# Performance work log

Measured on AMD Instinct MI355X. Metric: run time of the kernel, lower is better.

## Reference

```python
import jax, jax.numpy as jnp
import numpy as np

B, S, H, D, R = 16, 2048, 1024, 64, 2048  # batch, seq_len, hidden, inner_dim, num_relations


def setup_inputs() -> dict:
    key = jax.random.key(0)
    k1, k2, k3, k4 = jax.random.split(key, 4)
    last_hidden_state = jax.random.normal(k1, (B, S, H), dtype=jnp.float32)
    W = jax.random.normal(k2, (H, 2 * D), dtype=jnp.float32) * (H ** -0.5)
    b = jnp.zeros((2 * D,), dtype=jnp.float32)
    position_ids = jnp.tile(jnp.arange(S, dtype=jnp.int32), (B, 1))
    relations_idx = jax.random.randint(k3, (B, R, 4), 0, S, dtype=jnp.int32)
    labels_mask = (jax.random.uniform(k4, (B, R)) > 0.1).astype(jnp.float32)
    return {
        'last_hidden_state': last_hidden_state,
        'W': W,
        'b': b,
        'position_ids': position_ids,
        'relations_idx': relations_idx,
        'labels_mask': labels_mask,
    }


def reference(last_hidden_state, W, b, position_ids, relations_idx, labels_mask):
    # linear projection -> split into q/k halves
    outputs = last_hidden_state @ W + b            # [B,S,2D]
    qw, kw = outputs[..., :D], outputs[..., D:]    # each [B,S,D]

    # RoPE (interleaved sin/cos layout matching torch stack+reshape)
    inv_freq = jnp.power(10000.0, -2.0 * jnp.arange(D // 2, dtype=jnp.float32) / D)
    ang = position_ids[..., None].astype(jnp.float32) * inv_freq  # [B,S,D/2]
    sin_pos = jnp.repeat(jnp.sin(ang), 2, axis=-1)  # [B,S,D]
    cos_pos = jnp.repeat(jnp.cos(ang), 2, axis=-1)  # [B,S,D]

    def rotate(x):
        x2 = jnp.stack([-x[..., 1::2], x[..., ::2]], axis=-1).reshape(x.shape)
        return x * cos_pos + x2 * sin_pos

    qw = rotate(qw)
    kw = rotate(kw)

    # gather span endpoints: relations_idx[...,k] -> [B,R], take along seq axis
    def gather(x, idx):
        return jnp.take_along_axis(x, idx[..., None], axis=1)  # [B,R,D]

    sub_qw = jnp.concatenate([gather(qw, relations_idx[:, :, 0]),
                              gather(qw, relations_idx[:, :, 1])], axis=-1)  # [B,R,2D]
    obj_kw = jnp.concatenate([gather(kw, relations_idx[:, :, 2]),
                              gather(kw, relations_idx[:, :, 3])], axis=-1)  # [B,R,2D]

    logits = jnp.sum(sub_qw * obj_kw, axis=-1)     # [B,R]
    logits = logits + (1.0 - labels_mask) * -1e12
    return logits / jnp.sqrt(jnp.float32(D))
```

## Files before the change

### kernel.cpp

```cpp
#include <hip/hip_runtime.h>
#include <hip/hip_bf16.h>
#include <cstdint>

#define B_ 16
#define S_ 2048
#define H_ 1024
#define D_ 64
#define R_ 2048
#define M_ (B_*S_)
#define N_ 128
#define NC_ 16

typedef short short8 __attribute__((ext_vector_type(8)));
typedef float f32x4  __attribute__((ext_vector_type(4)));

__device__ __forceinline__ unsigned short f2bf(float f) {
    unsigned u = __builtin_bit_cast(unsigned, f);
    u += 0x7FFFu + ((u >> 16) & 1u);
    return (unsigned short)(u >> 16);
}
__device__ __forceinline__ unsigned pk2(float a, float b) {
    return (unsigned)f2bf(a) | ((unsigned)f2bf(b) << 16);
}
__device__ __forceinline__ float bflo(unsigned u) {
    return __builtin_bit_cast(float, u << 16);
}
__device__ __forceinline__ float bfhi(unsigned u) {
    return __builtin_bit_cast(float, u & 0xFFFF0000u);
}

typedef const __attribute__((address_space(1))) void gvoid_t;
typedef __attribute__((address_space(3))) void lvoid_t;
__device__ __forceinline__ void gload16(const void* g, void* l) {
    __builtin_amdgcn_global_load_lds((gvoid_t*)g, (lvoid_t*)l, 16, 0, 0);
}

__global__ void build_wt(const float* __restrict__ W, unsigned short* __restrict__ Wt) {
    __shared__ float tile[16][128];
    const int tid = threadIdx.x;
    const int k0  = blockIdx.x * 16;
    #pragma unroll
    for (int i = 0; i < 8; i++) {
        const int k = i * 2 + (tid >> 7);
        tile[k][tid & 127] = W[(size_t)(k0 + k) * N_ + (tid & 127)];
    }
    __syncthreads();
    const int n  = tid >> 1;
    const int kh = (tid & 1) * 8;
    short8 v;
    #pragma unroll
    for (int e = 0; e < 8; e++) v[e] = (short)f2bf(tile[kh + e][n]);
    *(short8*)(Wt + (size_t)n * 1024 + k0 + kh) = v;
}

__launch_bounds__(256, 2)
__global__ void gemm_rope(const float* __restrict__ A,
                          const unsigned short* __restrict__ Wt,
                          const float* __restrict__ bias,
                          const int* __restrict__ pos_ids,
                          unsigned* __restrict__ qk)
{
    __shared__ __align__(16) float          abuf[2][64 * 64];
    __shared__ __align__(16) unsigned short wbuf[2][N_ * 64];

    const int tid  = threadIdx.x;
    const int wave = tid >> 6, lane = tid & 63;
    const int ln15 = lane & 15, quad = lane >> 4, key = ln15 & 7;
    const int m0   = blockIdx.x * 64;

    const float* a_g[4];
    const unsigned short* w_g[4];
    int a_lo[4], w_lo[4];
    #pragma unroll
    for (int t = 0; t < 4; t++) {
        const int rl = wave * 16 + t * 4 + (lane >> 4);
        a_g[t]  = A + (size_t)(m0 + rl) * H_ + (((lane & 15) ^ (rl & 7)) << 2);
        a_lo[t] = (wave * 16 + t * 4) * 64;
        const int n = (wave * 4 + t) * 8 + (lane >> 3);
        w_g[t]  = Wt + (size_t)n * 1024 + (((lane & 7) ^ (n & 7)) << 3);
        w_lo[t] = (wave * 4 + t) * 8 * 64;
    }

    f32x4 acc[8];
    #pragma unroll
    for (int j = 0; j < 8; j++) acc[j] = (f32x4)0.f;

    #pragma unroll
    for (int t = 0; t < 4; t++) {
        gload16(a_g[t], &abuf[0][a_lo[t]]);
        gload16(w_g[t], &wbuf[0][w_lo[t]]);
    }

    const float* ab_lane_base;
    for (int kc = 0; kc < NC_; kc++) {
        __syncthreads();
        if (kc + 1 < NC_) {
            const int nb = (kc + 1) & 1;
            #pragma unroll
            for (int t = 0; t < 4; t++) {
                gload16(a_g[t] + (kc + 1) * 64, &abuf[nb][a_lo[t]]);
                gload16(w_g[t] + (kc + 1) * 64, &wbuf[nb][w_lo[t]]);
            }
        }
        const int cb = kc & 1;
        ab_lane_base = &abuf[cb][(wave * 16 + ln15) * 64];
        #pragma unroll
        for (int ks = 0; ks < 2; ks++) {
            const int g0 = ks * 8 + quad * 2;
            f32x4 r0 = *(const f32x4*)(ab_lane_base + ((g0 ^ key) << 2));
            f32x4 r1 = *(const f32x4*)(ab_lane_base + (((g0 + 1) ^ key) << 2));
            int4 ai;
            ai.x = (int)pk2(r0[0], r0[1]);
            ai.y = (int)pk2(r0[2], r0[3]);
            ai.z = (int)pk2(r1[0], r1[1]);
            ai.w = (int)pk2(r1[2], r1[3]);
            const short8 af = __builtin_bit_cast(short8, ai);
            const int p = ((ks * 4 + quad) ^ key) << 3;
            #pragma unroll
            for (int j = 0; j < 8; j++) {
                const short8 bf = *(const short8*)(&wbuf[cb][(j * 16 + ln15) * 64 + p]);
                acc[j] = __builtin_amdgcn_mfma_f32_16x16x32_bf16(af, bf, acc[j], 0, 0, 0);
            }
        }
    }

    const int rbase = m0 + wave * 16 + quad * 4;
    float bv[8], invr[4];
    #pragma unroll
    for (int j = 0; j < 8; j++) bv[j] = bias[j * 16 + ln15];
    #pragma unroll
    for (int jj = 0; jj < 4; jj++) {
        const float fi = (float)((jj * 16 + ln15) >> 1);
        invr[jj] = exp2f(fi * -0.41524101186092029f) * 0.15915494309189535f;
    }
    const bool odd = (ln15 & 1);
    #pragma unroll
    for (int reg = 0; reg < 4; reg++) {
        const int r = rbase + reg;
        const float pos = (float)pos_ids[r];
        float s_[4], c_[4];
        #pragma unroll
        for (int jj = 0; jj < 4; jj++) {
            const float fr = __builtin_amdgcn_fractf(pos * invr[jj]);
            s_[jj] = __builtin_amdgcn_sinf(fr);
            c_[jj] = __builtin_amdgcn_cosf(fr);
        }
        #pragma unroll
        for (int j = 0; j < 8; j++) {
            const int c = j * 16 + ln15;
            float v = acc[j][reg] + bv[j];
            float p = __shfl_xor(v, 1, 64);
            float outv = odd ? fmaf(v, c_[j & 3], p * s_[j & 3])
                             : fmaf(v, c_[j & 3], -p * s_[j & 3]);
            float po = __shfl_xor(outv, 1, 64);
            if (!odd)
                qk[(size_t)r * 64 + (c >> 1)] = pk2(outv, po);
        }
    }
}

__global__ void gather_dot(const unsigned* __restrict__ qk, const int* __restrict__ rel,
                           const float* __restrict__ mask, float* __restrict__ out)
{
    const int t    = blockIdx.x * 256 + threadIdx.x;
    const int w    = t >> 4;
    const int sub  = threadIdx.x & 15;
    const int b    = w >> 11;
    const int4 id4 = ((const int4*)rel)[w];
    const unsigned* base = qk + (size_t)b * S_ * 64;
    const int rq = (sub < 8) ? id4.x : id4.y;
    const int rk = (sub < 8) ? id4.z : id4.w;
    const int c4 = (sub & 7) * 4;
    const uint4 uq = *(const uint4*)(base + (size_t)rq * 64 + c4);
    const uint4 uk = *(const uint4*)(base + (size_t)rk * 64 + 32 + c4);
    float v;
    v  = bflo(uq.x) * bflo(uk.x) + bfhi(uq.x) * bfhi(uk.x);
    v += bflo(uq.y) * bflo(uk.y) + bfhi(uq.y) * bfhi(uk.y);
    v += bflo(uq.z) * bflo(uk.z) + bfhi(uq.z) * bfhi(uk.z);
    v += bflo(uq.w) * bflo(uk.w) + bfhi(uq.w) * bfhi(uk.w);
    #pragma unroll
    for (int off = 8; off; off >>= 1) v += __shfl_xor(v, off, 64);
    if (sub == 0)
        out[w] = (v + (1.0f - mask[w]) * -1e12f) * 0.125f;
}

extern "C" void kernel_launch(void* const* d_in, const int* in_sizes, int n_in,
                              void* d_out, int out_size, void* d_ws, size_t ws_size,
                              hipStream_t stream) {
    const float* lhs  = (const float*)d_in[0];
    const float* W    = (const float*)d_in[1];
    const float* bias = (const float*)d_in[2];
    const int*   pos  = (const int*)d_in[3];
    const int*   rel  = (const int*)d_in[4];
    const float* mask = (const float*)d_in[5];
    float* out = (float*)d_out;

    unsigned short* Wt = (unsigned short*)d_ws;
    unsigned* qk = (unsigned*)((char*)d_ws + (size_t)N_ * H_ * 2);

    build_wt<<<64, 256, 0, stream>>>(W, Wt);
    gemm_rope<<<512, 256, 0, stream>>>(lhs, Wt, bias, pos, qk);
    gather_dot<<<2048, 256, 0, stream>>>(qk, rel, mask, out);
}
```

Baseline: 214.4 us.

## Use 128-row tiles with 512 threads and a triple-buffered async load pipeline

After: 222.4 us. 3.7% more time.

```diff
diff --git a/kernel.cpp b/kernel.cpp
--- a/kernel.cpp
+++ b/kernel.cpp
@@ -53,32 +53,35 @@
     *(short8*)(Wt + (size_t)n * 1024 + k0 + kh) = v;
 }
 
-__launch_bounds__(256, 2)
+__launch_bounds__(512, 2)
 __global__ void gemm_rope(const float* __restrict__ A,
                           const unsigned short* __restrict__ Wt,
                           const float* __restrict__ bias,
                           const int* __restrict__ pos_ids,
                           unsigned* __restrict__ qk)
 {
-    __shared__ __align__(16) float          abuf[2][64 * 64];
-    __shared__ __align__(16) unsigned short wbuf[2][N_ * 64];
+    __shared__ __align__(16) float          abuf[3][128 * 64];
+    __shared__ __align__(16) unsigned short wbuf[3][N_ * 64];
 
     const int tid  = threadIdx.x;
     const int wave = tid >> 6, lane = tid & 63;
     const int ln15 = lane & 15, quad = lane >> 4, key = ln15 & 7;
-    const int m0   = blockIdx.x * 64;
+    const int m0   = blockIdx.x * 128;
 
     const float* a_g[4];
-    const unsigned short* w_g[4];
-    int a_lo[4], w_lo[4];
+    const unsigned short* w_g[2];
+    int a_lo[4], w_lo[2];
     #pragma unroll
     for (int t = 0; t < 4; t++) {
         const int rl = wave * 16 + t * 4 + (lane >> 4);
         a_g[t]  = A + (size_t)(m0 + rl) * H_ + (((lane & 15) ^ (rl & 7)) << 2);
         a_lo[t] = (wave * 16 + t * 4) * 64;
-        const int n = (wave * 4 + t) * 8 + (lane >> 3);
+    }
+    #pragma unroll
+    for (int t = 0; t < 2; t++) {
+        const int n = wave * 16 + t * 8 + (lane >> 3);
         w_g[t]  = Wt + (size_t)n * 1024 + (((lane & 7) ^ (n & 7)) << 3);
-        w_lo[t] = (wave * 4 + t) * 8 * 64;
+        w_lo[t] = (wave * 16 + t * 8) * 64;
     }
 
     f32x4 acc[8];
@@ -86,24 +89,33 @@
     for (int j = 0; j < 8; j++) acc[j] = (f32x4)0.f;
 
     #pragma unroll
-    for (int t = 0; t < 4; t++) {
-        gload16(a_g[t], &abuf[0][a_lo[t]]);
-        gload16(w_g[t], &wbuf[0][w_lo[t]]);
-    }
-
-    const float* ab_lane_base;
+    for (int t = 0; t < 4; t++) gload16(a_g[t],      &abuf[0][a_lo[t]]);
+    #pragma unroll
+    for (int t = 0; t < 2; t++) gload16(w_g[t],      &wbuf[0][w_lo[t]]);
+    #pragma unroll
+    for (int t = 0; t < 4; t++) gload16(a_g[t] + 64, &abuf[1][a_lo[t]]);
+    #pragma unroll
+    for (int t = 0; t < 2; t++) gload16(w_g[t] + 64, &wbuf[1][w_lo[t]]);
+
+    #pragma unroll 1
     for (int kc = 0; kc < NC_; kc++) {
-        __syncthreads();
-        if (kc + 1 < NC_) {
-            const int nb = (kc + 1) & 1;
+        if (kc + 2 < NC_) {
+            const int nb = (kc + 2) % 3;
             #pragma unroll
-            for (int t = 0; t < 4; t++) {
-                gload16(a_g[t] + (kc + 1) * 64, &abuf[nb][a_lo[t]]);
-                gload16(w_g[t] + (kc + 1) * 64, &wbuf[nb][w_lo[t]]);
-            }
-        }
-        const int cb = kc & 1;
-        ab_lane_base = &abuf[cb][(wave * 16 + ln15) * 64];
+            for (int t = 0; t < 4; t++) gload16(a_g[t] + (kc + 2) * 64, &abuf[nb][a_lo[t]]);
+            #pragma unroll
+            for (int t = 0; t < 2; t++) gload16(w_g[t] + (kc + 2) * 64, &wbuf[nb][w_lo[t]]);
+            asm volatile("s_waitcnt vmcnt(12)" ::: "memory");
+        } else if (kc + 1 < NC_) {
+            asm volatile("s_waitcnt vmcnt(6)" ::: "memory");
+        } else {
+            asm volatile("s_waitcnt vmcnt(0)" ::: "memory");
+        }
+        __builtin_amdgcn_sched_barrier(0);
+        __builtin_amdgcn_s_barrier();
+
+        const int cb = kc % 3;
+        const float* ab_lane_base = &abuf[cb][(wave * 16 + ln15) * 64];
         #pragma unroll
         for (int ks = 0; ks < 2; ks++) {
             const int g0 = ks * 8 + quad * 2;
@@ -122,6 +134,9 @@
                 acc[j] = __builtin_amdgcn_mfma_f32_16x16x32_bf16(af, bf, acc[j], 0, 0, 0);
             }
         }
+        asm volatile("s_waitcnt lgkmcnt(0)" ::: "memory");
+        __builtin_amdgcn_sched_barrier(0);
+        __builtin_amdgcn_s_barrier();
     }
 
     const int rbase = m0 + wave * 16 + quad * 4;
@@ -199,6 +214,6 @@
     unsigned* qk = (unsigned*)((char*)d_ws + (size_t)N_ * H_ * 2);
 
     build_wt<<<64, 256, 0, stream>>>(W, Wt);
-    gemm_rope<<<512, 256, 0, stream>>>(lhs, Wt, bias, pos, qk);
+    gemm_rope<<<256, 512, 0, stream>>>(lhs, Wt, bias, pos, qk);
     gather_dot<<<2048, 256, 0, stream>>>(qk, rel, mask, out);
 }
```

## Load A directly from global into registers and widen W k-chunks to 128

Applied to the files above, without the earlier changes.

New measurement: 220.0 us. 1.03x slower.

```diff
diff --git a/kernel.cpp b/kernel.cpp
--- a/kernel.cpp
+++ b/kernel.cpp
@@ -9,7 +9,7 @@
 #define R_ 2048
 #define M_ (B_*S_)
 #define N_ 128
-#define NC_ 16
+#define NCC_ 8
 
 typedef short short8 __attribute__((ext_vector_type(8)));
 typedef float f32x4  __attribute__((ext_vector_type(4)));
@@ -60,55 +60,44 @@
                           const int* __restrict__ pos_ids,
                           unsigned* __restrict__ qk)
 {
-    __shared__ __align__(16) float          abuf[2][64 * 64];
-    __shared__ __align__(16) unsigned short wbuf[2][N_ * 64];
+    __shared__ __align__(16) unsigned short wbuf[2][N_ * 128];
 
     const int tid  = threadIdx.x;
     const int wave = tid >> 6, lane = tid & 63;
     const int ln15 = lane & 15, quad = lane >> 4, key = ln15 & 7;
     const int m0   = blockIdx.x * 64;
 
-    const float* a_g[4];
-    const unsigned short* w_g[4];
-    int a_lo[4], w_lo[4];
+    const unsigned short* w_g[8];
+    int w_lo[8];
     #pragma unroll
-    for (int t = 0; t < 4; t++) {
-        const int rl = wave * 16 + t * 4 + (lane >> 4);
-        a_g[t]  = A + (size_t)(m0 + rl) * H_ + (((lane & 15) ^ (rl & 7)) << 2);
-        a_lo[t] = (wave * 16 + t * 4) * 64;
-        const int n = (wave * 4 + t) * 8 + (lane >> 3);
-        w_g[t]  = Wt + (size_t)n * 1024 + (((lane & 7) ^ (n & 7)) << 3);
-        w_lo[t] = (wave * 4 + t) * 8 * 64;
+    for (int t = 0; t < 8; t++) {
+        const int n = wave * 32 + t * 4 + (lane >> 4);
+        w_g[t]  = Wt + (size_t)n * 1024 + (((lane & 15) ^ (n & 7)) << 3);
+        w_lo[t] = (wave * 32 + t * 4) * 128;
     }
+
+    const float* Arow = A + (size_t)(m0 + wave * 16 + ln15) * H_ + quad * 8;
 
     f32x4 acc[8];
     #pragma unroll
     for (int j = 0; j < 8; j++) acc[j] = (f32x4)0.f;
 
     #pragma unroll
-    for (int t = 0; t < 4; t++) {
-        gload16(a_g[t], &abuf[0][a_lo[t]]);
-        gload16(w_g[t], &wbuf[0][w_lo[t]]);
-    }
+    for (int t = 0; t < 8; t++) gload16(w_g[t], &wbuf[0][w_lo[t]]);
 
-    const float* ab_lane_base;
-    for (int kc = 0; kc < NC_; kc++) {
+    #pragma unroll 1
+    for (int kc = 0; kc < NCC_; kc++) {
         __syncthreads();
-        if (kc + 1 < NC_) {
-            const int nb = (kc + 1) & 1;
+        if (kc + 1 < NCC_) {
             #pragma unroll
-            for (int t = 0; t < 4; t++) {
-                gload16(a_g[t] + (kc + 1) * 64, &abuf[nb][a_lo[t]]);
-                gload16(w_g[t] + (kc + 1) * 64, &wbuf[nb][w_lo[t]]);
-            }
+            for (int t = 0; t < 8; t++)
+                gload16(w_g[t] + (kc + 1) * 128, &wbuf[(kc + 1) & 1][w_lo[t]]);
         }
         const int cb = kc & 1;
-        ab_lane_base = &abuf[cb][(wave * 16 + ln15) * 64];
         #pragma unroll
-        for (int ks = 0; ks < 2; ks++) {
-            const int g0 = ks * 8 + quad * 2;
-            f32x4 r0 = *(const f32x4*)(ab_lane_base + ((g0 ^ key) << 2));
-            f32x4 r1 = *(const f32x4*)(ab_lane_base + (((g0 + 1) ^ key) << 2));
+        for (int ks = 0; ks < 4; ks++) {
+            f32x4 r0 = *(const f32x4*)(Arow + kc * 128 + ks * 32);
+            f32x4 r1 = *(const f32x4*)(Arow + kc * 128 + ks * 32 + 4);
             int4 ai;
             ai.x = (int)pk2(r0[0], r0[1]);
             ai.y = (int)pk2(r0[2], r0[3]);
@@ -118,7 +107,7 @@
             const int p = ((ks * 4 + quad) ^ key) << 3;
             #pragma unroll
             for (int j = 0; j < 8; j++) {
-                const short8 bf = *(const short8*)(&wbuf[cb][(j * 16 + ln15) * 64 + p]);
+                const short8 bf = *(const short8*)(&wbuf[cb][(j * 16 + ln15) * 128 + p]);
                 acc[j] = __builtin_amdgcn_mfma_f32_16x16x32_bf16(af, bf, acc[j], 0, 0, 0);
             }
         }
```
